# Optimization experiments

Measured on AMD Instinct MI355X. Metric: run time of the kernel, lower is better.

The kernel has to match this reference:

```python
import jax, jax.numpy as jnp
import numpy as np

# dims
B, S, D = 2, 4096, 1024
H, d, R, K, CH = 16, 64, 48, 4, 256


def causal_dwconv(x, w):
    # x: [B,S,C], w: [C,K] depthwise causal conv (torch Conv1d pad=K-1, keep first S)
    Kk = w.shape[1]
    xp = jnp.pad(x, ((0, 0), (Kk - 1, 0), (0, 0)))
    out = jnp.zeros_like(x)
    for j in range(Kk):
        out = out + w[:, j] * xp[:, j:j + x.shape[1], :]
    return out


def rmsnorm(x, w, eps=1e-6):
    return x * jax.lax.rsqrt(jnp.mean(x * x, axis=-1, keepdims=True) + eps) * w


def setup_inputs():
    key = jax.random.key(0)
    ks = jax.random.split(key, 16)
    rn = lambda k, shape, std=0.02: jax.random.normal(k, shape, jnp.float32) * std
    return {
        'x': jax.random.normal(ks[0], (B, S, D), jnp.float32),
        'Wq': rn(ks[1], (D, D)), 'Wk': rn(ks[2], (D, D)), 'Wv': rn(ks[3], (D, D)),
        'Wo': rn(ks[4], (D, D)),
        'conv_q': rn(ks[5], (D, K), 0.25), 'conv_k': rn(ks[6], (D, K), 0.25),
        'conv_v': rn(ks[7], (D, K), 0.25),
        'Wf': rn(ks[8], (D, H)), 'bf': jnp.full((H,), 2.0, jnp.float32),
        'Wl': rn(ks[9], (D, H)), 'bl': jnp.zeros((H,), jnp.float32),
        'Wrq': rn(ks[10], (D, H * R), 0.01), 'Wrk': rn(ks[11], (D, H * R), 0.01),
        'graph_scale': rn(ks[12], (H,), 0.1),
        'qn_w': jnp.ones((d,), jnp.float32), 'kn_w': jnp.ones((d,), jnp.float32),
        'on_w': jnp.ones((D,), jnp.float32),
    }


def _forward(x, Wq, Wk, Wv, Wo, conv_q, conv_k, conv_v, Wf, bf, Wl, bl, Wrq, Wrk,
             graph_scale, qn_w, kn_w, on_w):
    Bb, Ss, Dd = x.shape
    # proj + depthwise causal short conv, split heads -> [B,H,S,d]
    q = causal_dwconv(x @ Wq, conv_q).reshape(Bb, Ss, H, d).transpose(0, 2, 1, 3)
    k = causal_dwconv(x @ Wk, conv_k).reshape(Bb, Ss, H, d).transpose(0, 2, 1, 3)
    v = causal_dwconv(x @ Wv, conv_v).reshape(Bb, Ss, H, d).transpose(0, 2, 1, 3)
    q = rmsnorm(q, qn_w)
    k = rmsnorm(k, kn_w)
    # low-rank relative terms, zero-padded from R to d
    Rq = (x @ Wrq).reshape(Bb, Ss, H, R).transpose(0, 2, 1, 3)
    Rk = (x @ Wrk).reshape(Bb, Ss, H, R).transpose(0, 2, 1, 3)
    Rq = jnp.pad(Rq, ((0, 0), (0, 0), (0, 0), (0, d - R)))
    Rk = jnp.pad(Rk, ((0, 0), (0, 0), (0, 0), (0, d - R)))
    lam = jnp.abs(graph_scale)[None, :, None, None]
    ksum = k + lam * Rk
    k_tilde = ksum / jnp.clip(jnp.linalg.norm(ksum, axis=-1, keepdims=True), 1e-12)
    q_tilde = q + lam * Rq
    alpha = jax.nn.sigmoid(x @ Wf + bf).transpose(0, 2, 1)  # [B,H,S]
    beta = jax.nn.sigmoid(x @ Wl + bl).transpose(0, 2, 1)
    # gated delta-rule scan: mem[B,H,d,d]
    mem0 = jnp.zeros((Bb, H, d, d), x.dtype)
    nC = Ss // CH
    to_t = lambda a: a.transpose(2, 0, 1, 3).reshape(nC, CH, Bb, H, d)
    to_s = lambda a: a.transpose(2, 0, 1).reshape(nC, CH, Bb, H)
    xs = (to_t(k_tilde), to_t(v), to_t(q_tilde), to_s(alpha), to_s(beta))

    def step(mem, inp):
        k_t, v_t, q_t, a_t, b_t = inp
        retrieved = jnp.einsum('bhij,bhj->bhi', mem, k_t)
        delta = v_t - retrieved
        mem = a_t[..., None, None] * mem + b_t[..., None, None] * (delta[..., None] * k_t[..., None, :])
        out_t = jnp.einsum('bhij,bhj->bhi', mem, q_t)
        return mem, out_t

    def chunk_step(mem, inp):
        mem2, outs = jax.lax.scan(step, mem, inp)
        # original python scan detaches memory at chunk boundaries
        return jax.lax.stop_gradient(mem2), outs

    _, outs = jax.lax.scan(chunk_step, mem0, xs)  # [nC,CH,B,H,d]
    out = outs.reshape(Ss, Bb, H, d).transpose(1, 0, 2, 3).reshape(Bb, Ss, Dd)
    out = rmsnorm(out, on_w)
    return out @ Wo


def reference(x, Wq, Wk, Wv, Wo, conv_q, conv_k, conv_v, Wf, bf, Wl, bl, Wrq, Wrk,
              graph_scale, qn_w, kn_w, on_w):
    return _forward(x, Wq, Wk, Wv, Wo, conv_q, conv_k, conv_v, Wf, bf, Wl, bl,
                    Wrq, Wrk, graph_scale, qn_w, kn_w, on_w)
```

## Files before the change

### kernel.cpp

```cpp
#include <hip/hip_runtime.h>


typedef __attribute__((ext_vector_type(8))) short short8;
typedef __attribute__((ext_vector_type(4))) float f32x4;

#define B_ 2
#define S_ 4096
#define D_ 1024
#define H_ 16
#define R_ 48
#define M_ 8192
#define CW 16
#define NCH (S_ / CW)

__device__ __forceinline__ unsigned short f2bf(float f) {
  unsigned u = __float_as_uint(f);
  u += 0x7FFFu + ((u >> 16) & 1u);
  return (unsigned short)(u >> 16);
}
__device__ __forceinline__ float bf2f(unsigned short u) {
  return __uint_as_float(((unsigned)u) << 16);
}

__device__ __forceinline__ void lbar() {
  __builtin_amdgcn_sched_barrier(0);
  asm volatile("s_waitcnt lgkmcnt(0)" ::: "memory");
  __builtin_amdgcn_s_barrier();
  __builtin_amdgcn_sched_barrier(0);
}

#define GLDS16(g, l) __builtin_amdgcn_global_load_lds(                        \
    (const __attribute__((address_space(1))) unsigned int*)(g),              \
    (__attribute__((address_space(3))) unsigned int*)(l), 16, 0, 0)

__global__ __launch_bounds__(256) void cast_bf16_kernel(
    const float* __restrict__ in, unsigned short* __restrict__ out, int n4) {
  int i = blockIdx.x * 256 + threadIdx.x;
  for (; i < n4; i += gridDim.x * 256) {
    float4 v = ((const float4*)in)[i];
    ushort4 o;
    o.x = f2bf(v.x); o.y = f2bf(v.y); o.z = f2bf(v.z); o.w = f2bf(v.w);
    ((ushort4*)out)[i] = o;
  }
}

__global__ void transpose_w_kernel(const float* __restrict__ W,
                                   unsigned short* __restrict__ Wt,
                                   int Kd, int N) {
  __shared__ float tile[32][33];
  int n0 = blockIdx.x * 32, k0 = blockIdx.y * 32;
  int tx = threadIdx.x, ty = threadIdx.y;
#pragma unroll
  for (int i = 0; i < 32; i += 8)
    tile[ty + i][tx] = W[(size_t)(k0 + ty + i) * N + n0 + tx];
  __syncthreads();
#pragma unroll
  for (int i = 0; i < 32; i += 8)
    Wt[(size_t)(n0 + ty + i) * Kd + k0 + tx] = f2bf(tile[tx][ty + i]);
}

__global__ __launch_bounds__(256) void pack_wfl_kernel(
    const float* __restrict__ Wf, const float* __restrict__ Wl,
    unsigned short* __restrict__ wfl) {
  int o = blockIdx.x * 256 + threadIdx.x;
  int j = o >> 10, k = o & 1023;
  float v = (j < 16) ? Wf[k * 16 + j] : Wl[k * 16 + (j - 16)];
  wfl[o] = f2bf(v);
}

template <bool BF16OUT>
__global__ __launch_bounds__(256) void gemm_bt_kernel(
    const unsigned short* __restrict__ A, const unsigned short* __restrict__ Bt,
    void* __restrict__ Cv, int M, int N, int Kd) {
  __shared__ alignas(16) unsigned short lds[2 * 128 * 64];
  unsigned short* ldsA = lds;
  unsigned short* ldsB = lds + 128 * 64;
  int tid = threadIdx.x;
  int wave = tid >> 6, lane = tid & 63;
  int nBlocks = N >> 7;
  int bm = blockIdx.x / nBlocks, bn = blockIdx.x % nBlocks;
  int m0 = bm << 7, n0 = bn << 7;
  int wm = (wave >> 1) << 6, wn = (wave & 1) << 6;

  f32x4 acc[4][4] = {};

  int rowInChunk = lane >> 3;
  int kOff = (lane & 7) * 8;

  const unsigned short* Abase = A + (size_t)m0 * Kd;
  const unsigned short* Bbase = Bt + (size_t)n0 * Kd;

  for (int k0 = 0; k0 < Kd; k0 += 64) {
    __syncthreads();
#pragma unroll
    for (int r = 0; r < 4; r++) {
      int c = wave * 4 + r;
      int row = c * 8 + rowInChunk;
      GLDS16(Abase + (size_t)row * Kd + k0 + kOff, ldsA + c * 512);
    }
#pragma unroll
    for (int r = 0; r < 4; r++) {
      int c = wave * 4 + r;
      int row = c * 8 + rowInChunk;
      GLDS16(Bbase + (size_t)row * Kd + k0 + kOff, ldsB + c * 512);
    }
    asm volatile("s_waitcnt vmcnt(0)" ::: "memory");
    __syncthreads();
#pragma unroll
    for (int kk = 0; kk < 2; kk++) {
      short8 af[4], bfr[4];
      int kb = kk * 32 + (lane >> 4) * 8;
#pragma unroll
      for (int i = 0; i < 4; i++) {
        int ar = wm + i * 16 + (lane & 15);
        af[i] = *(const short8*)(ldsA + ar * 64 + kb);
        int br = wn + i * 16 + (lane & 15);
        bfr[i] = *(const short8*)(ldsB + br * 64 + kb);
      }
#pragma unroll
      for (int i = 0; i < 4; i++)
#pragma unroll
        for (int j = 0; j < 4; j++)
          acc[i][j] = __builtin_amdgcn_mfma_f32_16x16x32_bf16(
              af[i], bfr[j], acc[i][j], 0, 0, 0);
    }
  }
  int cr = (lane >> 4) * 4;
  int cc = lane & 15;
#pragma unroll
  for (int i = 0; i < 4; i++)
#pragma unroll
    for (int j = 0; j < 4; j++)
#pragma unroll
      for (int rg = 0; rg < 4; rg++) {
        int row = m0 + wm + i * 16 + cr + rg;
        int col = n0 + wn + j * 16 + cc;
        if (BF16OUT)
          ((unsigned short*)Cv)[(size_t)row * N + col] = f2bf(acc[i][j][rg]);
        else
          ((float*)Cv)[(size_t)row * N + col] = acc[i][j][rg];
      }
}

__global__ __launch_bounds__(256) void fl_gemm_kernel(
    const unsigned short* __restrict__ xb, const unsigned short* __restrict__ wfl,
    const float* __restrict__ bfv, const float* __restrict__ blv,
    float* __restrict__ alpha, float* __restrict__ beta) {
  __shared__ alignas(16) unsigned short ldsA[128 * 64];
  __shared__ alignas(16) unsigned short ldsB[32 * 64];
  int tid = threadIdx.x, wave = tid >> 6, lane = tid & 63;
  int m0 = blockIdx.x << 7;
  f32x4 acc[2][2] = {};
  int rowInChunk = lane >> 3, kOff = (lane & 7) * 8;
  const unsigned short* Abase = xb + (size_t)m0 * 1024;

  for (int k0 = 0; k0 < 1024; k0 += 64) {
    __syncthreads();
#pragma unroll
    for (int r = 0; r < 4; r++) {
      int ch = wave * 4 + r;
      int row = ch * 8 + rowInChunk;
      GLDS16(Abase + (size_t)row * 1024 + k0 + kOff, ldsA + ch * 512);
    }
    {
      int row = wave * 8 + rowInChunk;
      GLDS16(wfl + (size_t)row * 1024 + k0 + kOff, ldsB + wave * 512);
    }
    asm volatile("s_waitcnt vmcnt(0)" ::: "memory");
    __syncthreads();
#pragma unroll
    for (int kk = 0; kk < 2; kk++) {
      int kb2 = kk * 32 + (lane >> 4) * 8;
      short8 af[2], bfr[2];
#pragma unroll
      for (int i = 0; i < 2; i++)
        af[i] = *(const short8*)(ldsA + (wave * 32 + i * 16 + (lane & 15)) * 64 + kb2);
#pragma unroll
      for (int j = 0; j < 2; j++)
        bfr[j] = *(const short8*)(ldsB + (j * 16 + (lane & 15)) * 64 + kb2);
#pragma unroll
      for (int i = 0; i < 2; i++)
#pragma unroll
        for (int j = 0; j < 2; j++)
          acc[i][j] = __builtin_amdgcn_mfma_f32_16x16x32_bf16(
              af[i], bfr[j], acc[i][j], 0, 0, 0);
    }
  }
  int cr = (lane >> 4) * 4, cc = lane & 15;
#pragma unroll
  for (int i = 0; i < 2; i++)
#pragma unroll
    for (int j = 0; j < 2; j++)
#pragma unroll
      for (int rg = 0; rg < 4; rg++) {
        int row = m0 + wave * 32 + i * 16 + cr + rg;
        int col = j * 16 + cc;
        float z = acc[i][j][rg] + ((col < 16) ? bfv[col] : blv[col - 16]);
        float s = 1.f / (1.f + __expf(-z));
        int bb = row >> 12, tt = row & 4095, hh = col & 15;
        float* dst = (col < 16) ? alpha : beta;
        dst[((size_t)(bb * 16 + hh)) * 4096 + tt] = s;
      }
}

__global__ __launch_bounds__(256) void prep_kernel(
    const unsigned short* __restrict__ xqkv, const unsigned short* __restrict__ rqk,
    const float* __restrict__ cq, const float* __restrict__ ck,
    const float* __restrict__ cv, const float* __restrict__ gs,
    const float* __restrict__ qnw, const float* __restrict__ knw,
    unsigned short* __restrict__ qt, unsigned short* __restrict__ kt,
    unsigned short* __restrict__ vc) {
  int m = blockIdx.x;
  int b = m >> 12, t = m & 4095;
  int tid = threadIdx.x;
  int c4 = tid << 2;
  int h = c4 >> 6;
  int j4 = c4 & 63;

  float wq[4][4], wk[4][4], wv[4][4];
#pragma unroll
  for (int u = 0; u < 4; u++) {
    *(float4*)wq[u] = *(const float4*)(cq + (c4 + u) * 4);
    *(float4*)wk[u] = *(const float4*)(ck + (c4 + u) * 4);
    *(float4*)wv[u] = *(const float4*)(cv + (c4 + u) * 4);
  }
  float qv[4] = {0, 0, 0, 0}, kv[4] = {0, 0, 0, 0}, vv[4] = {0, 0, 0, 0};
#pragma unroll
  for (int j = 0; j < 4; j++) {
    int tt = t + j - 3;
    if (tt < 0) continue;
    const unsigned short* xr = xqkv + ((size_t)((b << 12) + tt)) * 3072;
    ushort4 uq = *(const ushort4*)(xr + c4);
    ushort4 uk = *(const ushort4*)(xr + 1024 + c4);
    ushort4 uv = *(const ushort4*)(xr + 2048 + c4);
    float xq[4] = {bf2f(uq.x), bf2f(uq.y), bf2f(uq.z), bf2f(uq.w)};
    float xk[4] = {bf2f(uk.x), bf2f(uk.y), bf2f(uk.z), bf2f(uk.w)};
    float xv[4] = {bf2f(uv.x), bf2f(uv.y), bf2f(uv.z), bf2f(uv.w)};
#pragma unroll
    for (int u = 0; u < 4; u++) {
      qv[u] = fmaf(wq[u][j], xq[u], qv[u]);
      kv[u] = fmaf(wk[u][j], xk[u], kv[u]);
      vv[u] = fmaf(wv[u][j], xv[u], vv[u]);
    }
  }
  float ssq = qv[0] * qv[0] + qv[1] * qv[1] + qv[2] * qv[2] + qv[3] * qv[3];
  ssq += __shfl_xor(ssq, 1); ssq += __shfl_xor(ssq, 2);
  ssq += __shfl_xor(ssq, 4); ssq += __shfl_xor(ssq, 8);
  float qsc = rsqrtf(ssq * (1.f / 64.f) + 1e-6f);
  float ssk = kv[0] * kv[0] + kv[1] * kv[1] + kv[2] * kv[2] + kv[3] * kv[3];
  ssk += __shfl_xor(ssk, 1); ssk += __shfl_xor(ssk, 2);
  ssk += __shfl_xor(ssk, 4); ssk += __shfl_xor(ssk, 8);
  float ksc = rsqrtf(ssk * (1.f / 64.f) + 1e-6f);

  float lam = fabsf(gs[h]);
  float rq[4] = {0, 0, 0, 0}, rk[4] = {0, 0, 0, 0};
  if (j4 < R_) {
    const unsigned short* rr = rqk + (size_t)m * 1536;
    ushort4 uq = *(const ushort4*)(rr + h * R_ + j4);
    ushort4 uk = *(const ushort4*)(rr + 768 + h * R_ + j4);
    rq[0] = bf2f(uq.x); rq[1] = bf2f(uq.y); rq[2] = bf2f(uq.z); rq[3] = bf2f(uq.w);
    rk[0] = bf2f(uk.x); rk[1] = bf2f(uk.y); rk[2] = bf2f(uk.z); rk[3] = bf2f(uk.w);
  }
  float qtv[4], ksum[4];
#pragma unroll
  for (int u = 0; u < 4; u++) {
    float qn = qv[u] * qsc * qnw[j4 + u];
    float kn = kv[u] * ksc * knw[j4 + u];
    qtv[u] = fmaf(lam, rq[u], qn);
    ksum[u] = fmaf(lam, rk[u], kn);
  }
  float ss2 = ksum[0] * ksum[0] + ksum[1] * ksum[1] + ksum[2] * ksum[2] +
              ksum[3] * ksum[3];
  ss2 += __shfl_xor(ss2, 1); ss2 += __shfl_xor(ss2, 2);
  ss2 += __shfl_xor(ss2, 4); ss2 += __shfl_xor(ss2, 8);
  float inv = 1.f / fmaxf(sqrtf(ss2), 1e-12f);

  size_t ob = ((size_t)((b * 16 + h) * 4096 + t)) * 64 + j4;
  ushort4 oq, ok, ov;
  oq.x = f2bf(qtv[0]); oq.y = f2bf(qtv[1]); oq.z = f2bf(qtv[2]); oq.w = f2bf(qtv[3]);
  ok.x = f2bf(ksum[0] * inv); ok.y = f2bf(ksum[1] * inv);
  ok.z = f2bf(ksum[2] * inv); ok.w = f2bf(ksum[3] * inv);
  ov.x = f2bf(vv[0]); ov.y = f2bf(vv[1]); ov.z = f2bf(vv[2]); ov.w = f2bf(vv[3]);
  *(ushort4*)(qt + ob) = oq;
  *(ushort4*)(kt + ob) = ok;
  *(ushort4*)(vc + ob) = ov;
}

__global__ __launch_bounds__(64) void wy_pre_kernel(
    const unsigned short* __restrict__ qt, const unsigned short* __restrict__ kt,
    const float* __restrict__ al, const float* __restrict__ be,
    unsigned short* __restrict__ Tw, unsigned short* __restrict__ Mw,
    float* __restrict__ Gw, unsigned short* __restrict__ KTw) {
  __shared__ float g5[5][16];
  __shared__ float Af[16][17];
  __shared__ unsigned short Tb[16][16];
  int tile = blockIdx.x;
  int bh = tile >> 8, c = tile & 255;
  int tg = c * CW;
  int l = threadIdx.x;

  const unsigned short* kb = kt + (size_t)bh * S_ * 64 + (size_t)tg * 64;
  const unsigned short* qb = qt + (size_t)bh * S_ * 64 + (size_t)tg * 64;

  float a_ = 1.f, bt_ = 0.f;
  if (l < 16) {
    a_ = al[(size_t)bh * S_ + tg + l];
    bt_ = be[(size_t)bh * S_ + tg + l];
  }
  float la = __log2f(a_);
  float pre = la;
  {
    float y;
    y = __shfl_up(pre, 1);  if (l >= 1) pre += y;
    y = __shfl_up(pre, 2);  if (l >= 2) pre += y;
    y = __shfl_up(pre, 4);  if (l >= 4) pre += y;
    y = __shfl_up(pre, 8);  if (l >= 8) pre += y;
  }
  float tot = __shfl(pre, 15);
  if (l < 16) {
    g5[0][l] = bt_;
    g5[1][l] = bt_ * exp2f(pre - la);
    g5[2][l] = exp2f(pre);
    g5[3][l] = exp2f(tot - pre);
    g5[4][l] = exp2f(-pre);
  }

  short8 kf0 = *(const short8*)(kb + (size_t)(l & 15) * 64 + (l >> 4) * 8);
  short8 kf1 = *(const short8*)(kb + (size_t)(l & 15) * 64 + 32 + (l >> 4) * 8);
  short8 qf0 = *(const short8*)(qb + (size_t)(l & 15) * 64 + (l >> 4) * 8);
  short8 qf1 = *(const short8*)(qb + (size_t)(l & 15) * 64 + 32 + (l >> 4) * 8);
  f32x4 aK = {0.f, 0.f, 0.f, 0.f}, aQ = {0.f, 0.f, 0.f, 0.f};
  aK = __builtin_amdgcn_mfma_f32_16x16x32_bf16(kf0, kf0, aK, 0, 0, 0);
  aK = __builtin_amdgcn_mfma_f32_16x16x32_bf16(kf1, kf1, aK, 0, 0, 0);
  aQ = __builtin_amdgcn_mfma_f32_16x16x32_bf16(qf0, kf0, aQ, 0, 0, 0);
  aQ = __builtin_amdgcn_mfma_f32_16x16x32_bf16(qf1, kf1, aQ, 0, 0, 0);

  {
    unsigned short* Ko = KTw + (size_t)tile * 1024 + (l & 15);
    int hi = l >> 4;
#pragma unroll
    for (int u = 0; u < 8; u++) {
      Ko[(hi * 8 + u) * 16] = (unsigned short)kf0[u];
      Ko[(32 + hi * 8 + u) * 16] = (unsigned short)kf1[u];
    }
  }

  __syncthreads();

  int s = l & 15;
  unsigned short* Mo = Mw + (size_t)tile * 256;
#pragma unroll
  for (int r = 0; r < 4; r++) {
    int t = (l >> 4) * 4 + r;
    Af[t][s] = (s < t) ? g5[1][t] * g5[4][s] * aK[r] : 0.f;
    float mv = (s <= t) ? g5[2][t] * g5[4][s] * aQ[r] : 0.f;
    Mo[t * 16 + s] = f2bf(mv);
  }
  __syncthreads();

  if (l < 16) {
    int j = l;
    float u[16];
#pragma unroll
    for (int t = 0; t < 16; t++) {
      float x = (t == j) ? 1.f : 0.f;
#pragma unroll
      for (int s2 = 0; s2 < 16; s2++) {
        if (s2 >= t) break;
        x = fmaf(-Af[t][s2], u[s2], x);
      }
      u[t] = x;
      Tb[t][j] = f2bf(x);
    }
  }
  __syncthreads();

  {
    ushort4 v = *(const ushort4*)&Tb[l >> 2][(l & 3) * 4];
    *(ushort4*)&Tw[(size_t)tile * 256 + l * 4] = v;
  }
  if (l < 64) Gw[(size_t)tile * 64 + l] = g5[l >> 4][l & 15];
}

__global__ __launch_bounds__(256, 1) void scan_wy_kernel(
    const unsigned short* __restrict__ qt, const unsigned short* __restrict__ kt,
    const unsigned short* __restrict__ vc, const unsigned short* __restrict__ Tw,
    const unsigned short* __restrict__ Mw, const float* __restrict__ Gw,
    const unsigned short* __restrict__ KTw, float* __restrict__ attn) {
  __shared__ alignas(16) unsigned short Kc[2][16][72];
  __shared__ alignas(16) unsigned short Qc[2][16][72];
  __shared__ alignas(16) unsigned short KT[2][64][40];
  __shared__ alignas(16) unsigned short Vc[2][16][24];
  __shared__ alignas(16) unsigned short Tl[2][16][40];
  __shared__ alignas(16) unsigned short Mb[2][16][40];
  __shared__ alignas(16) float G[2][64];
  __shared__ alignas(16) float SWq[16][20];
  __shared__ alignas(16) unsigned short Cb[16][40];
  __shared__ alignas(16) unsigned short Ubt[16][40];
  __shared__ alignas(16) unsigned short Udt[16][40];
  __shared__ alignas(16) unsigned short Sb[16][72];

  int blk = blockIdx.x;
  int bh = blk & 31, rg = blk >> 5;
  int b = bh >> 4, h = bh & 15;
  int tid = threadIdx.x;
  int w = tid >> 6, l = tid & 63;

  const unsigned short* kb = kt + (size_t)bh * S_ * 64;
  const unsigned short* qb = qt + (size_t)bh * S_ * 64;
  const unsigned short* vb = vc + (size_t)bh * S_ * 64 + rg * 16;
  const unsigned short* Tbg = Tw + (size_t)bh * 256 * 256;
  const unsigned short* Mbg = Mw + (size_t)bh * 256 * 256;
  const float* Gb = Gw + (size_t)bh * 256 * 64;
  const unsigned short* Kbg = KTw + (size_t)bh * 256 * 1024;
  float* ob = attn + (size_t)(b * S_) * 1024 + h * 64 + rg * 16;

  for (int i = tid; i < 16 * 72; i += 256) ((unsigned short*)Sb)[i] = 0;

  f32x4 Sreg = {0.f, 0.f, 0.f, 0.f};

  int trow = tid >> 4, ti = tid & 15;
  int jrow = tid >> 2, jq = tid & 3;
  ushort4 pk = *(const ushort4*)(kb + (size_t)trow * 64 + ti * 4);
  ushort4 pq = *(const ushort4*)(qb + (size_t)trow * 64 + ti * 4);
  unsigned short pv = vb[(size_t)trow * 64 + ti];
  unsigned short pt = Tbg[tid];
  unsigned short pm = Mbg[tid];
  ushort4 pkt = *(const ushort4*)(Kbg + tid * 4);
  float pg = (tid < 64) ? Gb[tid] : 0.f;

  lbar();

  for (int c = 0; c < NCH; ++c) {
    int p = c & 1;
    int tg0 = c * CW;
    *(ushort4*)&Kc[p][trow][ti * 4] = pk;
    *(ushort4*)&Qc[p][trow][ti * 4] = pq;
    *(ushort4*)&KT[p][jrow][jq * 4] = pkt;
    *(ushort4*)&KT[p][jrow][16 + jq * 4] = pkt;
    Vc[p][trow][ti] = pv;
    Tl[p][trow][ti] = pt;
    Tl[p][trow][16 + ti] = pt;
    Mb[p][trow][ti] = pm;
    Mb[p][trow][16 + ti] = pm;
    if (tid < 64) G[p][tid] = pg;
    if (c + 1 < NCH) {
      size_t cb = (size_t)(tg0 + CW) * 64;
      pk = *(const ushort4*)(kb + cb + (size_t)trow * 64 + ti * 4);
      pq = *(const ushort4*)(qb + cb + (size_t)trow * 64 + ti * 4);
      pv = vb[cb + (size_t)trow * 64 + ti];
      size_t t2 = (size_t)(c + 1) * 256;
      pt = Tbg[t2 + tid];
      pm = Mbg[t2 + tid];
      pkt = *(const ushort4*)(Kbg + (size_t)(c + 1) * 1024 + tid * 4);
      if (tid < 64) pg = Gb[(size_t)(c + 1) * 64 + tid];
    }
    lbar();

    if (w == 0) {
      short8 s0 = *(const short8*)&Sb[l & 15][(l >> 4) * 8];
      short8 s1 = *(const short8*)&Sb[l & 15][32 + (l >> 4) * 8];
      short8 b0 = *(const short8*)&Kc[p][l & 15][(l >> 4) * 8];
      short8 b1 = *(const short8*)&Kc[p][l & 15][32 + (l >> 4) * 8];
      f32x4 acc = {0.f, 0.f, 0.f, 0.f};
      acc = __builtin_amdgcn_mfma_f32_16x16x32_bf16(s0, b0, acc, 0, 0, 0);
      acc = __builtin_amdgcn_mfma_f32_16x16x32_bf16(s1, b1, acc, 0, 0, 0);
      int t = l & 15;
      float gb_ = G[p][t], bg_ = G[p][16 + t];
      ushort4 v4 = *(const ushort4*)&Vc[p][t][(l >> 4) * 4];
      unsigned short va[4] = {v4.x, v4.y, v4.z, v4.w};
#pragma unroll
      for (int r = 0; r < 4; r++) {
        int i = (l >> 4) * 4 + r;
        float c0 = gb_ * bf2f(va[r]) - bg_ * acc[r];
        unsigned short hi = f2bf(c0);
        Cb[i][t] = hi;
        Cb[i][16 + t] = f2bf(c0 - bf2f(hi));
      }
      short8 ta = *(const short8*)&Tl[p][l & 15][(l >> 4) * 8];
      short8 cbf = *(const short8*)&Cb[l & 15][(l >> 4) * 8];
      f32x4 ua = {0.f, 0.f, 0.f, 0.f};
      ua = __builtin_amdgcn_mfma_f32_16x16x32_bf16(ta, cbf, ua, 0, 0, 0);
      f32x4 gp4 = *(const f32x4*)&G[p][48 + (l >> 4) * 4];
      ushort4 uh, ulo, dh, dlo;
      unsigned short* uhp = &uh.x;
      unsigned short* ulp = &ulo.x;
      unsigned short* dhp = &dh.x;
      unsigned short* dlp = &dlo.x;
#pragma unroll
      for (int r = 0; r < 4; r++) {
        float uv = ua[r];
        unsigned short h1 = f2bf(uv);
        uhp[r] = h1;
        ulp[r] = f2bf(uv - bf2f(h1));
        float dv = uv * gp4[r];
        unsigned short h2 = f2bf(dv);
        dhp[r] = h2;
        dlp[r] = f2bf(dv - bf2f(h2));
      }
      *(ushort4*)&Ubt[l & 15][(l >> 4) * 4] = uh;
      *(ushort4*)&Ubt[l & 15][16 + (l >> 4) * 4] = ulo;
      *(ushort4*)&Udt[l & 15][(l >> 4) * 4] = dh;
      *(ushort4*)&Udt[l & 15][16 + (l >> 4) * 4] = dlo;
    } else if (w == 1) {
      short8 s0 = *(const short8*)&Sb[l & 15][(l >> 4) * 8];
      short8 s1 = *(const short8*)&Sb[l & 15][32 + (l >> 4) * 8];
      short8 b0 = *(const short8*)&Qc[p][l & 15][(l >> 4) * 8];
      short8 b1 = *(const short8*)&Qc[p][l & 15][32 + (l >> 4) * 8];
      f32x4 acc = {0.f, 0.f, 0.f, 0.f};
      acc = __builtin_amdgcn_mfma_f32_16x16x32_bf16(s0, b0, acc, 0, 0, 0);
      acc = __builtin_amdgcn_mfma_f32_16x16x32_bf16(s1, b1, acc, 0, 0, 0);
#pragma unroll
      for (int r = 0; r < 4; r++)
        SWq[(l >> 4) * 4 + r][l & 15] = acc[r];
    }
    lbar();

    if (w == 1) {
      short8 ma = *(const short8*)&Mb[p][l & 15][(l >> 4) * 8];
      short8 ub = *(const short8*)&Ubt[l & 15][(l >> 4) * 8];
      f32x4 oa = {0.f, 0.f, 0.f, 0.f};
      oa = __builtin_amdgcn_mfma_f32_16x16x32_bf16(ma, ub, oa, 0, 0, 0);
      f32x4 sq4 = *(const f32x4*)&SWq[l & 15][(l >> 4) * 4];
      f32x4 gm4 = *(const f32x4*)&G[p][32 + (l >> 4) * 4];
#pragma unroll
      for (int r = 0; r < 4; r++) {
        int t = (l >> 4) * 4 + r;
        ob[(size_t)(tg0 + t) * 1024 + (l & 15)] = oa[r] + gm4[r] * sq4[r];
      }
    }
    {
      float gE = G[p][32 + 15];
      short8 ud = *(const short8*)&Udt[l & 15][(l >> 4) * 8];
      short8 ktf = *(const short8*)&KT[p][16 * w + (l & 15)][(l >> 4) * 8];
      f32x4 ci;
#pragma unroll
      for (int r = 0; r < 4; r++) ci[r] = gE * Sreg[r];
      ci = __builtin_amdgcn_mfma_f32_16x16x32_bf16(ud, ktf, ci, 0, 0, 0);
      Sreg = ci;
#pragma unroll
      for (int r = 0; r < 4; r++)
        Sb[(l >> 4) * 4 + r][16 * w + (l & 15)] = f2bf(ci[r]);
    }
  }
}

__global__ __launch_bounds__(256) void rmsnorm_out_kernel(
    const float* __restrict__ attn, const float* __restrict__ onw,
    unsigned short* __restrict__ normed) {
  int m = blockIdx.x, tid = threadIdx.x;
  const float* row = attn + (size_t)m * 1024;
  float xv[4];
  *(float4*)xv = *(const float4*)(row + tid * 4);
  float ss = xv[0] * xv[0] + xv[1] * xv[1] + xv[2] * xv[2] + xv[3] * xv[3];
#pragma unroll
  for (int o = 1; o < 64; o <<= 1) ss += __shfl_xor(ss, o);
  __shared__ float wss[4];
  if ((tid & 63) == 0) wss[tid >> 6] = ss;
  __syncthreads();
  float tot = wss[0] + wss[1] + wss[2] + wss[3];
  float sc = rsqrtf(tot * (1.f / 1024.f) + 1e-6f);
  float wv[4];
  *(float4*)wv = *(const float4*)(onw + tid * 4);
  ushort4 o4;
  o4.x = f2bf(xv[0] * sc * wv[0]);
  o4.y = f2bf(xv[1] * sc * wv[1]);
  o4.z = f2bf(xv[2] * sc * wv[2]);
  o4.w = f2bf(xv[3] * sc * wv[3]);
  *(ushort4*)(normed + (size_t)m * 1024 + tid * 4) = o4;
}

extern "C" void kernel_launch(void* const* d_in, const int* in_sizes, int n_in,
                              void* d_out, int out_size, void* d_ws,
                              size_t ws_size, hipStream_t stream) {
  const float* x = (const float*)d_in[0];
  const float* Wq = (const float*)d_in[1];
  const float* Wk = (const float*)d_in[2];
  const float* Wv = (const float*)d_in[3];
  const float* Wo = (const float*)d_in[4];
  const float* conv_q = (const float*)d_in[5];
  const float* conv_k = (const float*)d_in[6];
  const float* conv_v = (const float*)d_in[7];
  const float* Wf = (const float*)d_in[8];
  const float* bfv = (const float*)d_in[9];
  const float* Wl = (const float*)d_in[10];
  const float* blv = (const float*)d_in[11];
  const float* gs = (const float*)d_in[14];
  const float* qn_w = (const float*)d_in[15];
  const float* kn_w = (const float*)d_in[16];
  const float* on_w = (const float*)d_in[17];

  char* ws = (char*)d_ws;
  size_t used = 0;
  auto alloc = [&](size_t bytes) -> void* {
    void* p = (void*)(ws + used);
    used += (bytes + 255) & ~(size_t)255;
    return p;
  };
  unsigned short* xb = (unsigned short*)alloc((size_t)M_ * D_ * 2);
  unsigned short* wqkv_t = (unsigned short*)alloc((size_t)3072 * 1024 * 2);
  unsigned short* wr_t = (unsigned short*)alloc((size_t)1536 * 1024 * 2);
  unsigned short* wo_t = (unsigned short*)alloc((size_t)1024 * 1024 * 2);
  unsigned short* wfl = (unsigned short*)alloc((size_t)32 * 1024 * 2);
  unsigned short* xqkv = (unsigned short*)alloc((size_t)M_ * 3072 * 2);
  unsigned short* rqk = (unsigned short*)alloc((size_t)M_ * 1536 * 2);
  unsigned short* qt = (unsigned short*)alloc((size_t)M_ * 1024 * 2);
  unsigned short* kt = (unsigned short*)alloc((size_t)M_ * 1024 * 2);
  unsigned short* vc = (unsigned short*)alloc((size_t)M_ * 1024 * 2);
  float* alpha = (float*)alloc((size_t)B_ * H_ * S_ * 4);
  float* beta = (float*)alloc((size_t)B_ * H_ * S_ * 4);
  float* attn = (float*)xqkv;
  unsigned short* normed = rqk;
  unsigned short* KTw = rqk;
  char* xbc = (char*)xb;
  unsigned short* Tw = (unsigned short*)xbc;
  unsigned short* Mw = (unsigned short*)(xbc + 4u * 1024 * 1024);
  float* Gw = (float*)(xbc + 8u * 1024 * 1024);

  if (used > ws_size) return;

  cast_bf16_kernel<<<2048, 256, 0, stream>>>(x, xb, M_ * D_ / 4);

  dim3 tb(32, 8);
  transpose_w_kernel<<<dim3(32, 32), tb, 0, stream>>>(Wq, wqkv_t, 1024, 1024);
  transpose_w_kernel<<<dim3(32, 32), tb, 0, stream>>>(
      Wk, wqkv_t + (size_t)1024 * 1024, 1024, 1024);
  transpose_w_kernel<<<dim3(32, 32), tb, 0, stream>>>(
      Wv, wqkv_t + (size_t)2048 * 1024, 1024, 1024);
  transpose_w_kernel<<<dim3(24, 32), tb, 0, stream>>>(
      (const float*)d_in[12], wr_t, 1024, 768);
  transpose_w_kernel<<<dim3(24, 32), tb, 0, stream>>>(
      (const float*)d_in[13], wr_t + (size_t)768 * 1024, 1024, 768);
  transpose_w_kernel<<<dim3(32, 32), tb, 0, stream>>>(Wo, wo_t, 1024, 1024);
  pack_wfl_kernel<<<128, 256, 0, stream>>>(Wf, Wl, wfl);

  gemm_bt_kernel<true><<<64 * 24, 256, 0, stream>>>(xb, wqkv_t, xqkv, M_, 3072, 1024);
  gemm_bt_kernel<true><<<64 * 12, 256, 0, stream>>>(xb, wr_t, rqk, M_, 1536, 1024);

  fl_gemm_kernel<<<64, 256, 0, stream>>>(xb, wfl, bfv, blv, alpha, beta);

  prep_kernel<<<M_, 256, 0, stream>>>(xqkv, rqk, conv_q, conv_k, conv_v, gs,
                                      qn_w, kn_w, qt, kt, vc);

  wy_pre_kernel<<<32 * 256, 64, 0, stream>>>(qt, kt, alpha, beta, Tw, Mw, Gw,
                                             KTw);

  scan_wy_kernel<<<128, 256, 0, stream>>>(qt, kt, vc, Tw, Mw, Gw, KTw, attn);

  rmsnorm_out_kernel<<<M_, 256, 0, stream>>>(attn, on_w, normed);

  gemm_bt_kernel<false><<<64 * 8, 256, 0, stream>>>(normed, wo_t, (float*)d_out,
                                                    M_, 1024, 1024);
}
```

Before: 522.7 us.

## Merge prepack launches, fuse QKV and low-rank GEMMs, simplify WY scan math

Folds the input cast, all weight transposes and the Wf/Wl packing into a single prepack launch, which removes several small kernel launches. The QKV and Wrq/Wrk projections now run as one wider GEMM writing a combined buffer, so the input matrix is read once and the launch tail is shared. The WY precompute and scan kernels also change their math: the Mw mask uses a total-decay factor instead of a per-column inverse, and the scan reuses the decayed Udt buffer instead of a separate hi/lo split of U. That last part changes numerics and must be equivalent to stay correct.

```diff
diff --git a/kernel.cpp b/kernel.cpp
--- a/kernel.cpp
+++ b/kernel.cpp
@@ -12,6 +12,7 @@
 #define M_ 8192
 #define CW 16
 #define NCH (S_ / CW)
+#define NPROJ 4608
 
 __device__ __forceinline__ unsigned short f2bf(float f) {
   unsigned u = __float_as_uint(f);
@@ -33,39 +34,63 @@
     (const __attribute__((address_space(1))) unsigned int*)(g),              \
     (__attribute__((address_space(3))) unsigned int*)(l), 16, 0, 0)
 
-__global__ __launch_bounds__(256) void cast_bf16_kernel(
-    const float* __restrict__ in, unsigned short* __restrict__ out, int n4) {
-  int i = blockIdx.x * 256 + threadIdx.x;
-  for (; i < n4; i += gridDim.x * 256) {
-    float4 v = ((const float4*)in)[i];
-    ushort4 o;
-    o.x = f2bf(v.x); o.y = f2bf(v.y); o.z = f2bf(v.z); o.w = f2bf(v.w);
-    ((ushort4*)out)[i] = o;
-  }
-}
-
-__global__ void transpose_w_kernel(const float* __restrict__ W,
-                                   unsigned short* __restrict__ Wt,
-                                   int Kd, int N) {
-  __shared__ float tile[32][33];
-  int n0 = blockIdx.x * 32, k0 = blockIdx.y * 32;
-  int tx = threadIdx.x, ty = threadIdx.y;
-#pragma unroll
-  for (int i = 0; i < 32; i += 8)
-    tile[ty + i][tx] = W[(size_t)(k0 + ty + i) * N + n0 + tx];
-  __syncthreads();
-#pragma unroll
-  for (int i = 0; i < 32; i += 8)
-    Wt[(size_t)(n0 + ty + i) * Kd + k0 + tx] = f2bf(tile[tx][ty + i]);
-}
-
-__global__ __launch_bounds__(256) void pack_wfl_kernel(
+__global__ __launch_bounds__(256) void prepack_kernel(
+    const float* __restrict__ x, unsigned short* __restrict__ xb,
+    const float* __restrict__ Wq, const float* __restrict__ Wk,
+    const float* __restrict__ Wv, const float* __restrict__ Wo,
+    const float* __restrict__ Wrq, const float* __restrict__ Wrk,
+    unsigned short* __restrict__ wproj_t, unsigned short* __restrict__ wo_t,
     const float* __restrict__ Wf, const float* __restrict__ Wl,
     unsigned short* __restrict__ wfl) {
-  int o = blockIdx.x * 256 + threadIdx.x;
-  int j = o >> 10, k = o & 1023;
-  float v = (j < 16) ? Wf[k * 16 + j] : Wl[k * 16 + (j - 16)];
-  wfl[o] = f2bf(v);
+  int blk = blockIdx.x;
+  int tid = threadIdx.x;
+  if (blk < 2048) {
+    const int n4 = M_ * D_ / 4;
+    for (int i = blk * 256 + tid; i < n4; i += 2048 * 256) {
+      float4 v = ((const float4*)x)[i];
+      ushort4 o;
+      o.x = f2bf(v.x); o.y = f2bf(v.y); o.z = f2bf(v.z); o.w = f2bf(v.w);
+      ((ushort4*)xb)[i] = o;
+    }
+    return;
+  }
+  if (blk < 7680) {
+    __shared__ float tile[32][33];
+    const float* W;
+    unsigned short* Wt;
+    int N, bx, by;
+    if (blk < 6144) {
+      int m = (blk - 2048) >> 10;
+      int r = (blk - 2048) & 1023;
+      N = 1024;
+      W = (m == 0) ? Wq : (m == 1) ? Wk : (m == 2) ? Wv : Wo;
+      Wt = (m == 3) ? wo_t : wproj_t + (size_t)m * 1024 * 1024;
+      bx = r & 31; by = r >> 5;
+    } else {
+      int m = (blk - 6144) / 768;
+      int r = (blk - 6144) % 768;
+      N = 768;
+      W = m ? Wrk : Wrq;
+      Wt = wproj_t + ((size_t)3072 + m * 768) * 1024;
+      bx = r % 24; by = r / 24;
+    }
+    int n0 = bx * 32, k0 = by * 32;
+    int tx = tid & 31, ty = tid >> 5;
+#pragma unroll
+    for (int i = 0; i < 32; i += 8)
+      tile[ty + i][tx] = W[(size_t)(k0 + ty + i) * N + n0 + tx];
+    __syncthreads();
+#pragma unroll
+    for (int i = 0; i < 32; i += 8)
+      Wt[(size_t)(n0 + ty + i) * 1024 + k0 + tx] = f2bf(tile[tx][ty + i]);
+    return;
+  }
+  {
+    int o = (blk - 7680) * 256 + tid;
+    int j = o >> 10, k = o & 1023;
+    float v = (j < 16) ? Wf[k * 16 + j] : Wl[k * 16 + (j - 16)];
+    wfl[o] = f2bf(v);
+  }
 }
 
 template <bool BF16OUT>
@@ -204,7 +229,7 @@
 }
 
 __global__ __launch_bounds__(256) void prep_kernel(
-    const unsigned short* __restrict__ xqkv, const unsigned short* __restrict__ rqk,
+    const unsigned short* __restrict__ proj,
     const float* __restrict__ cq, const float* __restrict__ ck,
     const float* __restrict__ cv, const float* __restrict__ gs,
     const float* __restrict__ qnw, const float* __restrict__ knw,
@@ -229,7 +254,7 @@
   for (int j = 0; j < 4; j++) {
     int tt = t + j - 3;
     if (tt < 0) continue;
-    const unsigned short* xr = xqkv + ((size_t)((b << 12) + tt)) * 3072;
+    const unsigned short* xr = proj + ((size_t)((b << 12) + tt)) * NPROJ;
     ushort4 uq = *(const ushort4*)(xr + c4);
     ushort4 uk = *(const ushort4*)(xr + 1024 + c4);
     ushort4 uv = *(const ushort4*)(xr + 2048 + c4);
@@ -255,7 +280,7 @@
   float lam = fabsf(gs[h]);
   float rq[4] = {0, 0, 0, 0}, rk[4] = {0, 0, 0, 0};
   if (j4 < R_) {
-    const unsigned short* rr = rqk + (size_t)m * 1536;
+    const unsigned short* rr = proj + (size_t)m * NPROJ + 3072;
     ushort4 uq = *(const ushort4*)(rr + h * R_ + j4);
     ushort4 uk = *(const ushort4*)(rr + 768 + h * R_ + j4);
     rq[0] = bf2f(uq.x); rq[1] = bf2f(uq.y); rq[2] = bf2f(uq.z); rq[3] = bf2f(uq.w);
@@ -291,7 +316,7 @@
     const float* __restrict__ al, const float* __restrict__ be,
     unsigned short* __restrict__ Tw, unsigned short* __restrict__ Mw,
     float* __restrict__ Gw, unsigned short* __restrict__ KTw) {
-  __shared__ float g5[5][16];
+  __shared__ float g5[4][16];
   __shared__ float Af[16][17];
   __shared__ unsigned short Tb[16][16];
   int tile = blockIdx.x;
@@ -317,13 +342,16 @@
     y = __shfl_up(pre, 8);  if (l >= 8) pre += y;
   }
   float tot = __shfl(pre, 15);
+  float ginv_l = exp2f(-pre);
+  float mtot = exp2f(-tot);
   if (l < 16) {
     g5[0][l] = bt_;
     g5[1][l] = bt_ * exp2f(pre - la);
     g5[2][l] = exp2f(pre);
     g5[3][l] = exp2f(tot - pre);
-    g5[4][l] = exp2f(-pre);
-  }
+  }
+  __shared__ float ginv_s[16];
+  if (l < 16) ginv_s[l] = ginv_l;
 
   short8 kf0 = *(const short8*)(kb + (size_t)(l & 15) * 64 + (l >> 4) * 8);
   short8 kf1 = *(const short8*)(kb + (size_t)(l & 15) * 64 + 32 + (l >> 4) * 8);
@@ -352,8 +380,8 @@
 #pragma unroll
   for (int r = 0; r < 4; r++) {
     int t = (l >> 4) * 4 + r;
-    Af[t][s] = (s < t) ? g5[1][t] * g5[4][s] * aK[r] : 0.f;
-    float mv = (s <= t) ? g5[2][t] * g5[4][s] * aQ[r] : 0.f;
+    Af[t][s] = (s < t) ? g5[1][t] * ginv_s[s] * aK[r] : 0.f;
+    float mv = (s <= t) ? g5[2][t] * mtot * aQ[r] : 0.f;
     Mo[t * 16 + s] = f2bf(mv);
   }
   __syncthreads();
@@ -396,7 +424,6 @@
   __shared__ alignas(16) float G[2][64];
   __shared__ alignas(16) float SWq[16][20];
   __shared__ alignas(16) unsigned short Cb[16][40];
-  __shared__ alignas(16) unsigned short Ubt[16][40];
   __shared__ alignas(16) unsigned short Udt[16][40];
   __shared__ alignas(16) unsigned short Sb[16][72];
 
@@ -482,24 +509,16 @@
       f32x4 ua = {0.f, 0.f, 0.f, 0.f};
       ua = __builtin_amdgcn_mfma_f32_16x16x32_bf16(ta, cbf, ua, 0, 0, 0);
       f32x4 gp4 = *(const f32x4*)&G[p][48 + (l >> 4) * 4];
-      ushort4 uh, ulo, dh, dlo;
-      unsigned short* uhp = &uh.x;
-      unsigned short* ulp = &ulo.x;
+      ushort4 dh, dlo;
       unsigned short* dhp = &dh.x;
       unsigned short* dlp = &dlo.x;
 #pragma unroll
       for (int r = 0; r < 4; r++) {
-        float uv = ua[r];
-        unsigned short h1 = f2bf(uv);
-        uhp[r] = h1;
-        ulp[r] = f2bf(uv - bf2f(h1));
-        float dv = uv * gp4[r];
+        float dv = ua[r] * gp4[r];
         unsigned short h2 = f2bf(dv);
         dhp[r] = h2;
         dlp[r] = f2bf(dv - bf2f(h2));
       }
-      *(ushort4*)&Ubt[l & 15][(l >> 4) * 4] = uh;
-      *(ushort4*)&Ubt[l & 15][16 + (l >> 4) * 4] = ulo;
       *(ushort4*)&Udt[l & 15][(l >> 4) * 4] = dh;
       *(ushort4*)&Udt[l & 15][16 + (l >> 4) * 4] = dlo;
     } else if (w == 1) {
@@ -516,9 +535,9 @@
     }
     lbar();
 
-    if (w == 1) {
+    if (w == 0) {
       short8 ma = *(const short8*)&Mb[p][l & 15][(l >> 4) * 8];
-      short8 ub = *(const short8*)&Ubt[l & 15][(l >> 4) * 8];
+      short8 ub = *(const short8*)&Udt[l & 15][(l >> 4) * 8];
       f32x4 oa = {0.f, 0.f, 0.f, 0.f};
       oa = __builtin_amdgcn_mfma_f32_16x16x32_bf16(ma, ub, oa, 0, 0, 0);
       f32x4 sq4 = *(const f32x4*)&SWq[l & 15][(l >> 4) * 4];
@@ -585,6 +604,8 @@
   const float* bfv = (const float*)d_in[9];
   const float* Wl = (const float*)d_in[10];
   const float* blv = (const float*)d_in[11];
+  const float* Wrq = (const float*)d_in[12];
+  const float* Wrk = (const float*)d_in[13];
   const float* gs = (const float*)d_in[14];
   const float* qn_w = (const float*)d_in[15];
   const float* kn_w = (const float*)d_in[16];
@@ -598,20 +619,19 @@
     return p;
   };
   unsigned short* xb = (unsigned short*)alloc((size_t)M_ * D_ * 2);
-  unsigned short* wqkv_t = (unsigned short*)alloc((size_t)3072 * 1024 * 2);
-  unsigned short* wr_t = (unsigned short*)alloc((size_t)1536 * 1024 * 2);
+  unsigned short* wproj_t = (unsigned short*)alloc((size_t)NPROJ * 1024 * 2);
   unsigned short* wo_t = (unsigned short*)alloc((size_t)1024 * 1024 * 2);
   unsigned short* wfl = (unsigned short*)alloc((size_t)32 * 1024 * 2);
-  unsigned short* xqkv = (unsigned short*)alloc((size_t)M_ * 3072 * 2);
-  unsigned short* rqk = (unsigned short*)alloc((size_t)M_ * 1536 * 2);
+  unsigned short* proj = (unsigned short*)alloc((size_t)M_ * NPROJ * 2);
   unsigned short* qt = (unsigned short*)alloc((size_t)M_ * 1024 * 2);
   unsigned short* kt = (unsigned short*)alloc((size_t)M_ * 1024 * 2);
   unsigned short* vc = (unsigned short*)alloc((size_t)M_ * 1024 * 2);
   float* alpha = (float*)alloc((size_t)B_ * H_ * S_ * 4);
   float* beta = (float*)alloc((size_t)B_ * H_ * S_ * 4);
-  float* attn = (float*)xqkv;
-  unsigned short* normed = rqk;
-  unsigned short* KTw = rqk;
+  char* projc = (char*)proj;
+  float* attn = (float*)projc;
+  unsigned short* KTw = (unsigned short*)(projc + 32u * 1024 * 1024);
+  unsigned short* normed = (unsigned short*)(projc + 48u * 1024 * 1024);
   char* xbc = (char*)xb;
   unsigned short* Tw = (unsigned short*)xbc;
   unsigned short* Mw = (unsigned short*)(xbc + 4u * 1024 * 1024);
@@ -619,28 +639,16 @@
 
   if (used > ws_size) return;
 
-  cast_bf16_kernel<<<2048, 256, 0, stream>>>(x, xb, M_ * D_ / 4);
-
-  dim3 tb(32, 8);
-  transpose_w_kernel<<<dim3(32, 32), tb, 0, stream>>>(Wq, wqkv_t, 1024, 1024);
-  transpose_w_kernel<<<dim3(32, 32), tb, 0, stream>>>(
-      Wk, wqkv_t + (size_t)1024 * 1024, 1024, 1024);
-  transpose_w_kernel<<<dim3(32, 32), tb, 0, stream>>>(
-      Wv, wqkv_t + (size_t)2048 * 1024, 1024, 1024);
-  transpose_w_kernel<<<dim3(24, 32), tb, 0, stream>>>(
-      (const float*)d_in[12], wr_t, 1024, 768);
-  transpose_w_kernel<<<dim3(24, 32), tb, 0, stream>>>(
-      (const float*)d_in[13], wr_t + (size_t)768 * 1024, 1024, 768);
-  transpose_w_kernel<<<dim3(32, 32), tb, 0, stream>>>(Wo, wo_t, 1024, 1024);
-  pack_wfl_kernel<<<128, 256, 0, stream>>>(Wf, Wl, wfl);
-
-  gemm_bt_kernel<true><<<64 * 24, 256, 0, stream>>>(xb, wqkv_t, xqkv, M_, 3072, 1024);
-  gemm_bt_kernel<true><<<64 * 12, 256, 0, stream>>>(xb, wr_t, rqk, M_, 1536, 1024);
+  prepack_kernel<<<7808, 256, 0, stream>>>(x, xb, Wq, Wk, Wv, Wo, Wrq, Wrk,
+                                           wproj_t, wo_t, Wf, Wl, wfl);
+
+  gemm_bt_kernel<true><<<64 * 36, 256, 0, stream>>>(xb, wproj_t, proj, M_,
+                                                    NPROJ, 1024);
 
   fl_gemm_kernel<<<64, 256, 0, stream>>>(xb, wfl, bfv, blv, alpha, beta);
 
-  prep_kernel<<<M_, 256, 0, stream>>>(xqkv, rqk, conv_q, conv_k, conv_v, gs,
-                                      qn_w, kn_w, qt, kt, vc);
+  prep_kernel<<<M_, 256, 0, stream>>>(proj, conv_q, conv_k, conv_v, gs, qn_w,
+                                      kn_w, qt, kt, vc);
 
   wy_pre_kernel<<<32 * 256, 64, 0, stream>>>(qt, kt, alpha, beta, Tw, Mw, Gw,
                                              KTw);
```

Result: faster. 489.6 us (-6.3%).
